# Optimization experiments

Hardware: AMD Instinct MI355X
Metric: run time of the kernel (lower is better)

Reference implementation:

```python
import jax, jax.numpy as jnp
import numpy as np

HEADS = 16
KV_HEADS = 4
HEAD_DIM = 64
HIDDEN = 1024
ROPE_THETA = 10000.0
NEG = -1e9


def _rope_cos_sin(seq_len, head_dim, dtype):
    inv_freq = 1.0 / (ROPE_THETA ** (jnp.arange(0, head_dim, 2, dtype=jnp.float32) / head_dim))
    pos = jnp.arange(seq_len, dtype=jnp.float32)
    freqs = jnp.outer(pos, inv_freq)                      # [S, d/2]
    emb = jnp.concatenate([freqs, freqs], axis=-1)        # [S, d]
    return jnp.cos(emb).astype(dtype), jnp.sin(emb).astype(dtype)


def _rotate_half(x):
    x1, x2 = jnp.split(x, 2, axis=-1)
    return jnp.concatenate([-x2, x1], axis=-1)


def setup_inputs() -> dict:
    key = jax.random.key(0)
    ks = jax.random.split(key, 5)
    B, S = 2, 2048
    hidden_states = jax.random.normal(ks[0], (B, S, HIDDEN), dtype=jnp.float32)
    # additive causal mask [1,1,S,S]
    causal = jnp.tril(jnp.ones((S, S), dtype=bool))
    attention_mask = jnp.where(causal, 0.0, NEG).astype(jnp.float32)[None, None]
    scale = 0.02
    Wq = jax.random.normal(ks[1], (HIDDEN, HEADS * HEAD_DIM), dtype=jnp.float32) * scale
    Wk = jax.random.normal(ks[2], (HIDDEN, KV_HEADS * HEAD_DIM), dtype=jnp.float32) * scale
    Wv = jax.random.normal(ks[3], (HIDDEN, KV_HEADS * HEAD_DIM), dtype=jnp.float32) * scale
    Wo = jax.random.normal(ks[4], (HEADS * HEAD_DIM, HIDDEN), dtype=jnp.float32) * scale
    return {"hidden_states": hidden_states, "attention_mask": attention_mask,
            "Wq": Wq, "Wk": Wk, "Wv": Wv, "Wo": Wo}


def reference(hidden_states, attention_mask, Wq, Wk, Wv, Wo):
    B, S, _ = hidden_states.shape
    G = HEADS // KV_HEADS  # kv groups

    q = (hidden_states @ Wq).reshape(B, S, HEADS, HEAD_DIM).transpose(0, 2, 1, 3)      # [B,H,S,d]
    k = (hidden_states @ Wk).reshape(B, S, KV_HEADS, HEAD_DIM).transpose(0, 2, 1, 3)   # [B,Hk,S,d]
    v = (hidden_states @ Wv).reshape(B, S, KV_HEADS, HEAD_DIM).transpose(0, 2, 1, 3)   # [B,Hk,S,d]

    cos, sin = _rope_cos_sin(S, HEAD_DIM, q.dtype)  # [S,d], broadcasts over B,H
    q = q * cos + _rotate_half(q) * sin
    k = k * cos + _rotate_half(k) * sin

    # GQA: query head h attends to kv head h // G (== repeat_interleave on kv heads)
    qg = q.reshape(B, KV_HEADS, G, S, HEAD_DIM)
    scores = jnp.einsum('bkgqd,bkld->bkgql', qg, k) / np.float32(np.sqrt(HEAD_DIM))  # [B,Hk,G,S,S]
    scores = scores + attention_mask[:, :, None, :, :]
    probs = jax.nn.softmax(scores.astype(jnp.float32), axis=-1).astype(q.dtype)
    out = jnp.einsum('bkgql,bkld->bkgqd', probs, v)            # [B,Hk,G,S,d]
    out = out.reshape(B, HEADS, S, HEAD_DIM).transpose(0, 2, 1, 3).reshape(B, S, HEADS * HEAD_DIM)
    return out @ Wo
```

## Files before the change

kernel.cpp:

```cpp
#include <hip/hip_runtime.h>
#include <hip/hip_bf16.h>
#include <math.h>

#define HEADS 16
#define KV_HEADS 4
#define HEAD_DIM 64
#define HIDDEN 1024
#define BATCH 2
#define SEQ 2048
#define ROWS (BATCH*SEQ)
#define NQKV (HEADS*HEAD_DIM + 2*KV_HEADS*HEAD_DIM)

typedef float f32x4 __attribute__((ext_vector_type(4)));
typedef __bf16 bf16x8 __attribute__((ext_vector_type(8)));
typedef int int4v __attribute__((ext_vector_type(4)));

static __device__ __forceinline__ unsigned short f2bf(float f) {
    union { float f; unsigned int u; } v; v.f = f;
    unsigned int r = v.u + 0x7fffu + ((v.u >> 16) & 1u);
    return (unsigned short)(r >> 16);
}

#define GLOAD_LDS16(gaddr, laddr) \
    __builtin_amdgcn_global_load_lds( \
        (const __attribute__((address_space(1))) unsigned int*)(gaddr), \
        (__attribute__((address_space(3))) unsigned int*)(laddr), 16, 0, 0)

__global__ void k_prep(const float* __restrict__ hs, unsigned short* __restrict__ hsb,
                       float* __restrict__ cosT, float* __restrict__ sinT) {
    int idx = blockIdx.x * blockDim.x + threadIdx.x;
    int stride = gridDim.x * blockDim.x;
    for (int i = idx; i < ROWS * HIDDEN / 4; i += stride) {
        float4 v = ((const float4*)hs)[i];
        hsb[i*4+0] = f2bf(v.x); hsb[i*4+1] = f2bf(v.y);
        hsb[i*4+2] = f2bf(v.z); hsb[i*4+3] = f2bf(v.w);
    }
    for (int i = idx; i < SEQ * 32; i += stride) {
        int s = i >> 5, f = i & 31;
        float inv = powf(10000.0f, -(float)f / 32.0f);
        float ang = (float)s * inv;
        cosT[i] = cosf(ang); sinT[i] = sinf(ang);
    }
}

__global__ __launch_bounds__(256) void k_wtrans(const float* __restrict__ Wq,
                                                const float* __restrict__ Wk,
                                                const float* __restrict__ Wv,
                                                const float* __restrict__ Wo,
                                                unsigned short* __restrict__ WqkvT,
                                                unsigned short* __restrict__ WoT) {
    __shared__ float tile[64][65];
    int bx = blockIdx.x;
    const float* src; unsigned short* dst; int ld, n0, k0;
    if (bx < 384) {
        int tn = bx % 24, tk = bx / 24;
        n0 = tn * 64; k0 = tk * 64; dst = WqkvT;
        if (n0 < 1024)      { src = Wq + n0;          ld = 1024; }
        else if (n0 < 1280) { src = Wk + (n0 - 1024); ld = 256;  }
        else                { src = Wv + (n0 - 1280); ld = 256;  }
    } else {
        int i2 = bx - 384;
        int tn = i2 & 15, tk = i2 >> 4;
        n0 = tn * 64; k0 = tk * 64;
        src = Wo + n0; ld = 1024; dst = WoT;
    }
    int tx = threadIdx.x & 63, ty = threadIdx.x >> 6;
#pragma unroll
    for (int j = 0; j < 16; j++) {
        int k = j * 4 + ty;
        tile[k][tx] = src[(size_t)(k0 + k) * ld + tx];
    }
    __syncthreads();
#pragma unroll
    for (int j = 0; j < 16; j++) {
        int r = j * 4 + ty;
        dst[(size_t)(n0 + r) * 1024 + k0 + tx] = f2bf(tile[tx][r]);
    }
}

template <bool BF16_OUT>
__global__ __launch_bounds__(256) void k_gemm(const unsigned short* __restrict__ A,
                                              const unsigned short* __restrict__ Bt,
                                              void* __restrict__ Cv,
                                              int M, int N, int K) {
    __shared__ unsigned short lA[128*64];
    __shared__ unsigned short lB[128*64];
    const int tid = threadIdx.x;
    const int lane = tid & 63;
    const int wid = tid >> 6;
    const int wr = wid >> 1, wc = wid & 1;
    const int m0 = blockIdx.y * 128;
    const int n0 = blockIdx.x * 128;
    const int l15 = lane & 15, lq = lane >> 4;

    f32x4 acc[4][4];
#pragma unroll
    for (int i = 0; i < 4; i++)
#pragma unroll
        for (int j = 0; j < 4; j++) acc[i][j] = (f32x4){0.f,0.f,0.f,0.f};

    for (int k0 = 0; k0 < K; k0 += 64) {
        __syncthreads();
#pragma unroll
        for (int it = 0; it < 4; ++it) {
            int c = tid + it * 256;
            int row = c >> 3, slot = c & 7;
            int gs = slot ^ (row & 7);
            GLOAD_LDS16(A + (size_t)(m0 + row) * K + k0 + gs * 8, (char*)lA + c * 16);
            GLOAD_LDS16(Bt + (size_t)(n0 + row) * K + k0 + gs * 8, (char*)lB + c * 16);
        }
        __syncthreads();
#pragma unroll
        for (int t = 0; t < 2; t++) {
            bf16x8 af[4], bfr[4];
#pragma unroll
            for (int i = 0; i < 4; i++) {
                int row = wr * 64 + i * 16 + l15;
                int slot = (t * 4 + lq) ^ (row & 7);
                af[i] = *(const bf16x8*)((const char*)lA + row * 128 + slot * 16);
            }
#pragma unroll
            for (int j = 0; j < 4; j++) {
                int row = wc * 64 + j * 16 + l15;
                int slot = (t * 4 + lq) ^ (row & 7);
                bfr[j] = *(const bf16x8*)((const char*)lB + row * 128 + slot * 16);
            }
#pragma unroll
            for (int i = 0; i < 4; i++)
#pragma unroll
                for (int j = 0; j < 4; j++)
                    acc[i][j] = __builtin_amdgcn_mfma_f32_16x16x32_bf16(af[i], bfr[j], acc[i][j], 0, 0, 0);
        }
    }
#pragma unroll
    for (int i = 0; i < 4; i++) {
#pragma unroll
        for (int j = 0; j < 4; j++) {
            int col = n0 + wc * 64 + j * 16 + l15;
#pragma unroll
            for (int r = 0; r < 4; r++) {
                int row = m0 + wr * 64 + i * 16 + lq * 4 + r;
                if constexpr (BF16_OUT)
                    ((unsigned short*)Cv)[(size_t)row * N + col] = f2bf(acc[i][j][r]);
                else
                    ((float*)Cv)[(size_t)row * N + col] = acc[i][j][r];
            }
        }
    }
}

__global__ void k_rope(const unsigned short* __restrict__ QKVb,
                       const float* __restrict__ cosT, const float* __restrict__ sinT,
                       unsigned short* __restrict__ Kb) {
    int idx = blockIdx.x * blockDim.x + threadIdx.x;
    int stride = gridDim.x * blockDim.x;
    for (int i = idx; i < ROWS * KV_HEADS * 4; i += stride) {
        int c = i & 3, hk = (i >> 2) & 3, row = i >> 4;
        int b = row >> 11, s = row & 2047;
        int f0 = c * 8;
        const unsigned short* base = QKVb + (size_t)row * NQKV + 1024 + hk * 64;
        bf16x8 lo = *(const bf16x8*)(base + f0);
        bf16x8 hi = *(const bf16x8*)(base + 32 + f0);
        f32x4 c0 = *(const f32x4*)(cosT + s * 32 + f0);
        f32x4 c1 = *(const f32x4*)(cosT + s * 32 + f0 + 4);
        f32x4 s0 = *(const f32x4*)(sinT + s * 32 + f0);
        f32x4 s1 = *(const f32x4*)(sinT + s * 32 + f0 + 4);
        bf16x8 rlo, rhi;
#pragma unroll
        for (int e = 0; e < 8; e++) {
            float cc = (e < 4) ? c0[e] : c1[e - 4];
            float ss = (e < 4) ? s0[e] : s1[e - 4];
            float k1 = (float)lo[e], k2 = (float)hi[e];
            rlo[e] = (__bf16)(k1 * cc - k2 * ss);
            rhi[e] = (__bf16)(k2 * cc + k1 * ss);
        }
        size_t o = ((size_t)(b * KV_HEADS + hk) * SEQ + s) * 64 + f0;
        *(bf16x8*)(Kb + o)      = rlo;
        *(bf16x8*)(Kb + o + 32) = rhi;
    }
}

__global__ __launch_bounds__(256) void k_vtrans(const unsigned short* __restrict__ QKVb,
                                                unsigned short* __restrict__ Vt) {
    __shared__ unsigned short tile[64][66];
    int s0 = blockIdx.x * 64;
    int bhk = blockIdx.y;
    int b = bhk >> 2, hk = bhk & 3;
    int t = threadIdx.x;
    int r = t >> 3, c = t & 7;
    const unsigned short* base = QKVb + (size_t)b * SEQ * NQKV + 1280 + hk * 64;
#pragma unroll
    for (int rr = r; rr < 64; rr += 32) {
        unsigned short tmp[8];
        *(int4v*)tmp = *(const int4v*)(base + (size_t)(s0 + rr) * NQKV + c * 8);
#pragma unroll
        for (int e = 0; e < 8; e++) tile[rr][c * 8 + e] = tmp[e];
    }
    __syncthreads();
    unsigned short* outb = Vt + (size_t)bhk * 64 * SEQ;
#pragma unroll
    for (int dd = r; dd < 64; dd += 32) {
        unsigned short tmp[8];
#pragma unroll
        for (int e = 0; e < 8; e++) tmp[e] = tile[c * 8 + e][dd];
        *(int4v*)(outb + (size_t)dd * SEQ + s0 + c * 8) = *(int4v*)tmp;
    }
}

__global__ __launch_bounds__(256) void k_attn(const unsigned short* __restrict__ QKVb,
                                              const unsigned short* __restrict__ Kb,
                                              const unsigned short* __restrict__ Vt,
                                              const float* __restrict__ cosT,
                                              const float* __restrict__ sinT,
                                              unsigned short* __restrict__ Ob) {
    __shared__ unsigned short lK[2][64*64];
    __shared__ unsigned short lV[2][64*64];
    __shared__ unsigned short lP[4][16*64];
    const int tid = threadIdx.x;
    const int lane = tid & 63;
    const int w = tid >> 6;
    const int l15 = lane & 15, lq = lane >> 4;
    const int bh = blockIdx.x;
    const int qt = (int)gridDim.y - 1 - (int)blockIdx.y;
    const int b = bh >> 4, h = bh & 15;
    const int hk = h >> 2;
    const int q0 = qt * 64;

    bf16x8 aq[2];
    {
        int s = q0 + w * 16 + l15;
        const unsigned short* Qp = QKVb + (size_t)(b * SEQ + s) * NQKV + h * 64;
        bf16x8 lo = *(const bf16x8*)(Qp + lq * 8);
        bf16x8 hi = *(const bf16x8*)(Qp + 32 + lq * 8);
        const float* cp = cosT + s * 32 + lq * 8;
        const float* sp = sinT + s * 32 + lq * 8;
        f32x4 c0 = *(const f32x4*)cp, c1 = *(const f32x4*)(cp + 4);
        f32x4 s0 = *(const f32x4*)sp, s1 = *(const f32x4*)(sp + 4);
        bf16x8 rlo, rhi;
#pragma unroll
        for (int jj = 0; jj < 8; jj++) {
            float c  = (jj < 4) ? c0[jj] : c1[jj - 4];
            float sn = (jj < 4) ? s0[jj] : s1[jj - 4];
            float q1 = (float)lo[jj], q2 = (float)hi[jj];
            rlo[jj] = (__bf16)((q1 * c - q2 * sn) * 0.125f);
            rhi[jj] = (__bf16)((q2 * c + q1 * sn) * 0.125f);
        }
        aq[0] = rlo; aq[1] = rhi;
    }

    f32x4 oacc[4];
    float mrun[4], lrun[4];
#pragma unroll
    for (int d = 0; d < 4; d++) {
        oacc[d] = (f32x4){0.f,0.f,0.f,0.f};
        mrun[d] = -INFINITY; lrun[d] = 0.f;
    }

    const unsigned short* Kg = Kb + (size_t)(b * KV_HEADS + hk) * SEQ * 64;
    const unsigned short* Vg = Vt + (size_t)(b * KV_HEADS + hk) * 64 * SEQ;

#define STAGE_KV(buf, kv0)                                                        \
    {                                                                             \
        _Pragma("unroll")                                                         \
        for (int it = 0; it < 2; ++it) {                                          \
            int c = tid + it * 256;                                               \
            int row = c >> 3, slot = c & 7;                                       \
            int gs = slot ^ (row & 7);                                            \
            GLOAD_LDS16(Kg + (size_t)((kv0) + row) * 64 + gs * 8,                 \
                        (char*)lK[buf] + c * 16);                                 \
            GLOAD_LDS16(Vg + (size_t)row * SEQ + (kv0) + gs * 8,                  \
                        (char*)lV[buf] + c * 16);                                 \
        }                                                                         \
    }

    STAGE_KV(0, 0);
    __syncthreads();
    int cur = 0;

    for (int j = 0; j <= qt; ++j) {
        if (j < qt) STAGE_KV(cur ^ 1, (j + 1) * 64);

        int kv0 = j * 64;
        f32x4 sf[4];
#pragma unroll
        for (int kb = 0; kb < 4; kb++) {
            sf[kb] = (f32x4){0.f,0.f,0.f,0.f};
#pragma unroll
            for (int t = 0; t < 2; t++) {
                int row = kb * 16 + l15;
                int slot = (t * 4 + lq) ^ (row & 7);
                bf16x8 bk = *(const bf16x8*)((const char*)lK[cur] + row * 128 + slot * 16);
                sf[kb] = __builtin_amdgcn_mfma_f32_16x16x32_bf16(aq[t], bk, sf[kb], 0, 0, 0);
            }
        }
        if (j == qt) {
#pragma unroll
            for (int kb = 0; kb < 4; kb++)
#pragma unroll
                for (int r = 0; r < 4; r++) {
                    int kv = kv0 + kb * 16 + l15;
                    int q = q0 + w * 16 + lq * 4 + r;
                    if (kv > q) sf[kb][r] = -INFINITY;
                }
        }
#pragma unroll
        for (int r = 0; r < 4; r++) {
            float m = fmaxf(fmaxf(sf[0][r], sf[1][r]), fmaxf(sf[2][r], sf[3][r]));
            m = fmaxf(m, __shfl_xor(m, 1));
            m = fmaxf(m, __shfl_xor(m, 2));
            m = fmaxf(m, __shfl_xor(m, 4));
            m = fmaxf(m, __shfl_xor(m, 8));
            if (__any(m > mrun[r])) {
                float newm = fmaxf(mrun[r], m);
                float fac = __expf(mrun[r] - newm);
                mrun[r] = newm;
                lrun[r] *= fac;
#pragma unroll
                for (int d = 0; d < 4; d++) oacc[d][r] *= fac;
            }
            float rs = 0.f;
#pragma unroll
            for (int kb = 0; kb < 4; kb++) {
                float p = __expf(sf[kb][r] - mrun[r]);
                sf[kb][r] = p; rs += p;
            }
            rs += __shfl_xor(rs, 1); rs += __shfl_xor(rs, 2);
            rs += __shfl_xor(rs, 4); rs += __shfl_xor(rs, 8);
            lrun[r] += rs;
        }
        unsigned short* lPw = lP[w];
#pragma unroll
        for (int kb = 0; kb < 4; kb++)
#pragma unroll
            for (int r = 0; r < 4; r++) {
                int q = lq * 4 + r;
                int kv = kb * 16 + l15;
                int byte = (q * 128 + kv * 2) ^ ((q & 7) << 4);
                *(unsigned short*)((char*)lPw + byte) = f2bf(sf[kb][r]);
            }
#pragma unroll
        for (int t = 0; t < 2; t++) {
            int qr = l15;
            int slota = (t * 4 + lq) ^ (qr & 7);
            bf16x8 ap = *(const bf16x8*)((const char*)lPw + qr * 128 + slota * 16);
#pragma unroll
            for (int db = 0; db < 4; db++) {
                int vrow = db * 16 + l15;
                int slotv = (t * 4 + lq) ^ (vrow & 7);
                bf16x8 bv = *(const bf16x8*)((const char*)lV[cur] + vrow * 128 + slotv * 16);
                oacc[db] = __builtin_amdgcn_mfma_f32_16x16x32_bf16(ap, bv, oacc[db], 0, 0, 0);
            }
        }
        __syncthreads();
        cur ^= 1;
    }
    float linv[4];
#pragma unroll
    for (int r = 0; r < 4; r++) linv[r] = 1.0f / lrun[r];
#pragma unroll
    for (int db = 0; db < 4; db++)
#pragma unroll
        for (int r = 0; r < 4; r++) {
            int q = q0 + w * 16 + lq * 4 + r;
            int col = h * 64 + db * 16 + l15;
            Ob[((size_t)b * SEQ + q) * 1024 + col] = f2bf(oacc[db][r] * linv[r]);
        }
#undef STAGE_KV
}

extern "C" void kernel_launch(void* const* d_in, const int* in_sizes, int n_in,
                              void* d_out, int out_size, void* d_ws, size_t ws_size,
                              hipStream_t stream) {
    const float* hs = (const float*)d_in[0];
    const float* Wq = (const float*)d_in[2];
    const float* Wk = (const float*)d_in[3];
    const float* Wv = (const float*)d_in[4];
    const float* Wo = (const float*)d_in[5];
    float* out = (float*)d_out;

    char* ws = (char*)d_ws;
    unsigned short* hsb   = (unsigned short*)ws; ws += (size_t)ROWS * HIDDEN * 2;
    unsigned short* WqkvT = (unsigned short*)ws; ws += (size_t)NQKV * HIDDEN * 2;
    unsigned short* WoT   = (unsigned short*)ws; ws += (size_t)HIDDEN * HIDDEN * 2;
    float* cosT = (float*)ws; ws += (size_t)SEQ * 32 * 4;
    float* sinT = (float*)ws; ws += (size_t)SEQ * 32 * 4;
    unsigned short* QKVb = (unsigned short*)ws; ws += (size_t)ROWS * NQKV * 2;
    unsigned short* Kb = (unsigned short*)ws; ws += (size_t)BATCH * KV_HEADS * SEQ * 64 * 2;
    unsigned short* Vt = (unsigned short*)ws; ws += (size_t)BATCH * KV_HEADS * 64 * SEQ * 2;
    unsigned short* Ob = (unsigned short*)ws; ws += (size_t)ROWS * HIDDEN * 2;

    k_prep<<<1024, 256, 0, stream>>>(hs, hsb, cosT, sinT);
    k_wtrans<<<640, 256, 0, stream>>>(Wq, Wk, Wv, Wo, WqkvT, WoT);

    dim3 g1(NQKV / 128, ROWS / 128);
    k_gemm<true><<<g1, 256, 0, stream>>>(hsb, WqkvT, QKVb, ROWS, NQKV, HIDDEN);

    k_rope<<<256, 256, 0, stream>>>(QKVb, cosT, sinT, Kb);
    k_vtrans<<<dim3(SEQ / 64, BATCH * KV_HEADS), 256, 0, stream>>>(QKVb, Vt);

    dim3 ga(BATCH * HEADS, SEQ / 64);
    k_attn<<<ga, 256, 0, stream>>>(QKVb, Kb, Vt, cosT, sinT, Ob);

    dim3 g2(HIDDEN / 128, ROWS / 128);
    k_gemm<false><<<g2, 256, 0, stream>>>(Ob, WoT, out, ROWS, HIDDEN, HIDDEN);
}
```

Before: 217.0 us.

## Fuse RoPE and softmax scale into QKV GEMM epilogue, merge prep kernels

Applies rotary embedding and the Q scale (1/sqrt(d)·log2e) in the QKV GEMM epilogue. This removes the separate k_rope kernel, the Kb buffer, and the per-block Q RoPE in attention. Attention now reads K straight from the strided QKV buffer and uses exp2f with the folded log2e scale. The two prep kernels are merged into one launch. Costs: strided K loads in attention and more work in the GEMM epilogue.

```diff
diff --git a/kernel.cpp b/kernel.cpp
--- a/kernel.cpp
+++ b/kernel.cpp
@@ -10,6 +10,7 @@
 #define SEQ 2048
 #define ROWS (BATCH*SEQ)
 #define NQKV (HEADS*HEAD_DIM + 2*KV_HEADS*HEAD_DIM)
+#define QSCL 0.1803368867f
 
 typedef float f32x4 __attribute__((ext_vector_type(4)));
 typedef __bf16 bf16x8 __attribute__((ext_vector_type(8)));
@@ -26,62 +27,67 @@
         (const __attribute__((address_space(1))) unsigned int*)(gaddr), \
         (__attribute__((address_space(3))) unsigned int*)(laddr), 16, 0, 0)
 
-__global__ void k_prep(const float* __restrict__ hs, unsigned short* __restrict__ hsb,
-                       float* __restrict__ cosT, float* __restrict__ sinT) {
-    int idx = blockIdx.x * blockDim.x + threadIdx.x;
-    int stride = gridDim.x * blockDim.x;
-    for (int i = idx; i < ROWS * HIDDEN / 4; i += stride) {
-        float4 v = ((const float4*)hs)[i];
-        hsb[i*4+0] = f2bf(v.x); hsb[i*4+1] = f2bf(v.y);
-        hsb[i*4+2] = f2bf(v.z); hsb[i*4+3] = f2bf(v.w);
-    }
-    for (int i = idx; i < SEQ * 32; i += stride) {
-        int s = i >> 5, f = i & 31;
-        float inv = powf(10000.0f, -(float)f / 32.0f);
-        float ang = (float)s * inv;
-        cosT[i] = cosf(ang); sinT[i] = sinf(ang);
-    }
-}
-
-__global__ __launch_bounds__(256) void k_wtrans(const float* __restrict__ Wq,
-                                                const float* __restrict__ Wk,
-                                                const float* __restrict__ Wv,
-                                                const float* __restrict__ Wo,
-                                                unsigned short* __restrict__ WqkvT,
-                                                unsigned short* __restrict__ WoT) {
+__global__ __launch_bounds__(256) void k_fprep(const float* __restrict__ hs,
+                                               const float* __restrict__ Wq,
+                                               const float* __restrict__ Wk,
+                                               const float* __restrict__ Wv,
+                                               const float* __restrict__ Wo,
+                                               unsigned short* __restrict__ hsb,
+                                               unsigned short* __restrict__ WqkvT,
+                                               unsigned short* __restrict__ WoT,
+                                               float* __restrict__ cosT,
+                                               float* __restrict__ sinT) {
     __shared__ float tile[64][65];
     int bx = blockIdx.x;
-    const float* src; unsigned short* dst; int ld, n0, k0;
-    if (bx < 384) {
-        int tn = bx % 24, tk = bx / 24;
-        n0 = tn * 64; k0 = tk * 64; dst = WqkvT;
-        if (n0 < 1024)      { src = Wq + n0;          ld = 1024; }
-        else if (n0 < 1280) { src = Wk + (n0 - 1024); ld = 256;  }
-        else                { src = Wv + (n0 - 1280); ld = 256;  }
+    if (bx < 640) {
+        const float* src; unsigned short* dst; int ld, n0, k0;
+        if (bx < 384) {
+            int tn = bx % 24, tk = bx / 24;
+            n0 = tn * 64; k0 = tk * 64; dst = WqkvT;
+            if (n0 < 1024)      { src = Wq + n0;          ld = 1024; }
+            else if (n0 < 1280) { src = Wk + (n0 - 1024); ld = 256;  }
+            else                { src = Wv + (n0 - 1280); ld = 256;  }
+        } else {
+            int i2 = bx - 384;
+            int tn = i2 & 15, tk = i2 >> 4;
+            n0 = tn * 64; k0 = tk * 64;
+            src = Wo + n0; ld = 1024; dst = WoT;
+        }
+        int tx = threadIdx.x & 63, ty = threadIdx.x >> 6;
+#pragma unroll
+        for (int j = 0; j < 16; j++) {
+            int k = j * 4 + ty;
+            tile[k][tx] = src[(size_t)(k0 + k) * ld + tx];
+        }
+        __syncthreads();
+#pragma unroll
+        for (int j = 0; j < 16; j++) {
+            int r = j * 4 + ty;
+            dst[(size_t)(n0 + r) * 1024 + k0 + tx] = f2bf(tile[tx][r]);
+        }
     } else {
-        int i2 = bx - 384;
-        int tn = i2 & 15, tk = i2 >> 4;
-        n0 = tn * 64; k0 = tk * 64;
-        src = Wo + n0; ld = 1024; dst = WoT;
-    }
-    int tx = threadIdx.x & 63, ty = threadIdx.x >> 6;
-#pragma unroll
-    for (int j = 0; j < 16; j++) {
-        int k = j * 4 + ty;
-        tile[k][tx] = src[(size_t)(k0 + k) * ld + tx];
-    }
-    __syncthreads();
-#pragma unroll
-    for (int j = 0; j < 16; j++) {
-        int r = j * 4 + ty;
-        dst[(size_t)(n0 + r) * 1024 + k0 + tx] = f2bf(tile[tx][r]);
-    }
-}
-
-template <bool BF16_OUT>
+        int idx = (bx - 640) * 256 + threadIdx.x;
+        int stride = 384 * 256;
+        for (int i = idx; i < ROWS * HIDDEN / 4; i += stride) {
+            float4 v = ((const float4*)hs)[i];
+            hsb[i*4+0] = f2bf(v.x); hsb[i*4+1] = f2bf(v.y);
+            hsb[i*4+2] = f2bf(v.z); hsb[i*4+3] = f2bf(v.w);
+        }
+        for (int i = idx; i < SEQ * 32; i += stride) {
+            int s = i >> 5, f = i & 31;
+            float inv = powf(10000.0f, -(float)f / 32.0f);
+            float ang = (float)s * inv;
+            cosT[i] = cosf(ang); sinT[i] = sinf(ang);
+        }
+    }
+}
+
+template <bool BF16_OUT, bool ROPE>
 __global__ __launch_bounds__(256) void k_gemm(const unsigned short* __restrict__ A,
                                               const unsigned short* __restrict__ Bt,
                                               void* __restrict__ Cv,
+                                              const float* __restrict__ cosT,
+                                              const float* __restrict__ sinT,
                                               int M, int N, int K) {
     __shared__ unsigned short lA[128*64];
     __shared__ unsigned short lB[128*64];
@@ -132,6 +138,32 @@
                     acc[i][j] = __builtin_amdgcn_mfma_f32_16x16x32_bf16(af[i], bfr[j], acc[i][j], 0, 0, 0);
         }
     }
+    if constexpr (ROPE) {
+        const int hc0 = n0 + wc * 64;
+        if (hc0 < 1280) {
+            const float scl = (hc0 < 1024) ? QSCL : 1.0f;
+#pragma unroll
+            for (int i = 0; i < 4; i++) {
+#pragma unroll
+                for (int r = 0; r < 4; r++) {
+                    int row = m0 + wr * 64 + i * 16 + lq * 4 + r;
+                    int s = row & (SEQ - 1);
+                    float c_lo = cosT[s * 32 + l15],      c_hi = cosT[s * 32 + 16 + l15];
+                    float s_lo = sinT[s * 32 + l15],      s_hi = sinT[s * 32 + 16 + l15];
+#pragma unroll
+                    for (int j = 0; j < 4; j++) {
+                        float c  = (j & 1) ? c_hi : c_lo;
+                        float sn = (j & 1) ? s_hi : s_lo;
+                        float v = acc[i][j][r], vp = acc[i][j ^ 2][r];
+                        float o = (j < 2) ? (v * c - vp * sn) : (v * c + vp * sn);
+                        int col = n0 + wc * 64 + j * 16 + l15;
+                        ((unsigned short*)Cv)[(size_t)row * N + col] = f2bf(o * scl);
+                    }
+                }
+            }
+            return;
+        }
+    }
 #pragma unroll
     for (int i = 0; i < 4; i++) {
 #pragma unroll
@@ -146,37 +178,6 @@
                     ((float*)Cv)[(size_t)row * N + col] = acc[i][j][r];
             }
         }
-    }
-}
-
-__global__ void k_rope(const unsigned short* __restrict__ QKVb,
-                       const float* __restrict__ cosT, const float* __restrict__ sinT,
-                       unsigned short* __restrict__ Kb) {
-    int idx = blockIdx.x * blockDim.x + threadIdx.x;
-    int stride = gridDim.x * blockDim.x;
-    for (int i = idx; i < ROWS * KV_HEADS * 4; i += stride) {
-        int c = i & 3, hk = (i >> 2) & 3, row = i >> 4;
-        int b = row >> 11, s = row & 2047;
-        int f0 = c * 8;
-        const unsigned short* base = QKVb + (size_t)row * NQKV + 1024 + hk * 64;
-        bf16x8 lo = *(const bf16x8*)(base + f0);
-        bf16x8 hi = *(const bf16x8*)(base + 32 + f0);
-        f32x4 c0 = *(const f32x4*)(cosT + s * 32 + f0);
-        f32x4 c1 = *(const f32x4*)(cosT + s * 32 + f0 + 4);
-        f32x4 s0 = *(const f32x4*)(sinT + s * 32 + f0);
-        f32x4 s1 = *(const f32x4*)(sinT + s * 32 + f0 + 4);
-        bf16x8 rlo, rhi;
-#pragma unroll
-        for (int e = 0; e < 8; e++) {
-            float cc = (e < 4) ? c0[e] : c1[e - 4];
-            float ss = (e < 4) ? s0[e] : s1[e - 4];
-            float k1 = (float)lo[e], k2 = (float)hi[e];
-            rlo[e] = (__bf16)(k1 * cc - k2 * ss);
-            rhi[e] = (__bf16)(k2 * cc + k1 * ss);
-        }
-        size_t o = ((size_t)(b * KV_HEADS + hk) * SEQ + s) * 64 + f0;
-        *(bf16x8*)(Kb + o)      = rlo;
-        *(bf16x8*)(Kb + o + 32) = rhi;
     }
 }
 
@@ -208,10 +209,7 @@
 }
 
 __global__ __launch_bounds__(256) void k_attn(const unsigned short* __restrict__ QKVb,
-                                              const unsigned short* __restrict__ Kb,
                                               const unsigned short* __restrict__ Vt,
-                                              const float* __restrict__ cosT,
-                                              const float* __restrict__ sinT,
                                               unsigned short* __restrict__ Ob) {
     __shared__ unsigned short lK[2][64*64];
     __shared__ unsigned short lV[2][64*64];
@@ -230,22 +228,8 @@
     {
         int s = q0 + w * 16 + l15;
         const unsigned short* Qp = QKVb + (size_t)(b * SEQ + s) * NQKV + h * 64;
-        bf16x8 lo = *(const bf16x8*)(Qp + lq * 8);
-        bf16x8 hi = *(const bf16x8*)(Qp + 32 + lq * 8);
-        const float* cp = cosT + s * 32 + lq * 8;
-        const float* sp = sinT + s * 32 + lq * 8;
-        f32x4 c0 = *(const f32x4*)cp, c1 = *(const f32x4*)(cp + 4);
-        f32x4 s0 = *(const f32x4*)sp, s1 = *(const f32x4*)(sp + 4);
-        bf16x8 rlo, rhi;
-#pragma unroll
-        for (int jj = 0; jj < 8; jj++) {
-            float c  = (jj < 4) ? c0[jj] : c1[jj - 4];
-            float sn = (jj < 4) ? s0[jj] : s1[jj - 4];
-            float q1 = (float)lo[jj], q2 = (float)hi[jj];
-            rlo[jj] = (__bf16)((q1 * c - q2 * sn) * 0.125f);
-            rhi[jj] = (__bf16)((q2 * c + q1 * sn) * 0.125f);
-        }
-        aq[0] = rlo; aq[1] = rhi;
+        aq[0] = *(const bf16x8*)(Qp + lq * 8);
+        aq[1] = *(const bf16x8*)(Qp + 32 + lq * 8);
     }
 
     f32x4 oacc[4];
@@ -256,7 +240,7 @@
         mrun[d] = -INFINITY; lrun[d] = 0.f;
     }
 
-    const unsigned short* Kg = Kb + (size_t)(b * KV_HEADS + hk) * SEQ * 64;
+    const unsigned short* Kg = QKVb + (size_t)b * SEQ * NQKV + 1024 + hk * 64;
     const unsigned short* Vg = Vt + (size_t)(b * KV_HEADS + hk) * 64 * SEQ;
 
 #define STAGE_KV(buf, kv0)                                                        \
@@ -266,7 +250,7 @@
             int c = tid + it * 256;                                               \
             int row = c >> 3, slot = c & 7;                                       \
             int gs = slot ^ (row & 7);                                            \
-            GLOAD_LDS16(Kg + (size_t)((kv0) + row) * 64 + gs * 8,                 \
+            GLOAD_LDS16(Kg + (size_t)((kv0) + row) * NQKV + gs * 8,               \
                         (char*)lK[buf] + c * 16);                                 \
             GLOAD_LDS16(Vg + (size_t)row * SEQ + (kv0) + gs * 8,                  \
                         (char*)lV[buf] + c * 16);                                 \
@@ -312,7 +296,7 @@
             m = fmaxf(m, __shfl_xor(m, 8));
             if (__any(m > mrun[r])) {
                 float newm = fmaxf(mrun[r], m);
-                float fac = __expf(mrun[r] - newm);
+                float fac = exp2f(mrun[r] - newm);
                 mrun[r] = newm;
                 lrun[r] *= fac;
 #pragma unroll
@@ -321,7 +305,7 @@
             float rs = 0.f;
 #pragma unroll
             for (int kb = 0; kb < 4; kb++) {
-                float p = __expf(sf[kb][r] - mrun[r]);
+                float p = exp2f(sf[kb][r] - mrun[r]);
                 sf[kb][r] = p; rs += p;
             }
             rs += __shfl_xor(rs, 1); rs += __shfl_xor(rs, 2);
@@ -336,7 +320,7 @@
                 int q = lq * 4 + r;
                 int kv = kb * 16 + l15;
                 int byte = (q * 128 + kv * 2) ^ ((q & 7) << 4);
-                *(unsigned short*)((char*)lPw + byte) = f2bf(sf[kb][r]);
+                *(__bf16*)((char*)lPw + byte) = (__bf16)sf[kb][r];
             }
 #pragma unroll
         for (int t = 0; t < 2; t++) {
@@ -385,22 +369,19 @@
     float* cosT = (float*)ws; ws += (size_t)SEQ * 32 * 4;
     float* sinT = (float*)ws; ws += (size_t)SEQ * 32 * 4;
     unsigned short* QKVb = (unsigned short*)ws; ws += (size_t)ROWS * NQKV * 2;
-    unsigned short* Kb = (unsigned short*)ws; ws += (size_t)BATCH * KV_HEADS * SEQ * 64 * 2;
     unsigned short* Vt = (unsigned short*)ws; ws += (size_t)BATCH * KV_HEADS * 64 * SEQ * 2;
     unsigned short* Ob = (unsigned short*)ws; ws += (size_t)ROWS * HIDDEN * 2;
 
-    k_prep<<<1024, 256, 0, stream>>>(hs, hsb, cosT, sinT);
-    k_wtrans<<<640, 256, 0, stream>>>(Wq, Wk, Wv, Wo, WqkvT, WoT);
+    k_fprep<<<1024, 256, 0, stream>>>(hs, Wq, Wk, Wv, Wo, hsb, WqkvT, WoT, cosT, sinT);
 
     dim3 g1(NQKV / 128, ROWS / 128);
-    k_gemm<true><<<g1, 256, 0, stream>>>(hsb, WqkvT, QKVb, ROWS, NQKV, HIDDEN);
-
-    k_rope<<<256, 256, 0, stream>>>(QKVb, cosT, sinT, Kb);
+    k_gemm<true, true><<<g1, 256, 0, stream>>>(hsb, WqkvT, QKVb, cosT, sinT, ROWS, NQKV, HIDDEN);
+
     k_vtrans<<<dim3(SEQ / 64, BATCH * KV_HEADS), 256, 0, stream>>>(QKVb, Vt);
 
     dim3 ga(BATCH * HEADS, SEQ / 64);
-    k_attn<<<ga, 256, 0, stream>>>(QKVb, Kb, Vt, cosT, sinT, Ob);
+    k_attn<<<ga, 256, 0, stream>>>(QKVb, Vt, Ob);
 
     dim3 g2(HIDDEN / 128, ROWS / 128);
-    k_gemm<false><<<g2, 256, 0, stream>>>(Ob, WoT, out, ROWS, HIDDEN, HIDDEN);
-}
+    k_gemm<false, false><<<g2, 256, 0, stream>>>(Ob, WoT, out, nullptr, nullptr, ROWS, HIDDEN, HIDDEN);
+}
```

Result: no change. 217.0 us (-0.0%).
